# Kernel tuning notes

Hardware: AMD Instinct MI355X
Metric: run time of the kernel (lower is better)

## Reference

```python
import jax, jax.numpy as jnp
import numpy as np


def setup_inputs() -> dict:
    key = jax.random.key(0)
    k1, k2, k3, k4, k5 = jax.random.split(key, 5)
    B, S, IN, OUT, GS = 64, 1, 8192, 28672, 128
    n_groups = IN // GS  # 64
    return {
        "input": jax.random.normal(k1, (B, S, IN), dtype=jnp.float32),
        # packed int4 weights: two 4-bit values per byte along in_features
        "qweight": jax.random.randint(k2, (IN // 2, OUT), 0, 256, dtype=jnp.int32),
        # per-group scales (small positive, typical of quantized weights)
        "scales": (jax.random.uniform(k3, (n_groups, OUT), dtype=jnp.float32) * 0.01 + 1e-3),
        # per-group zero points, 4-bit range
        "qzeros": jax.random.randint(k4, (n_groups, OUT), 0, 16, dtype=jnp.int32),
        "bias": jax.random.normal(k5, (OUT,), dtype=jnp.float32),
        "group_size": GS,
    }


def _dequant_int4(qweight, scales, qzeros, group_size):
    # qweight: [in/2, out] bytes; low nibble = even k, high nibble = odd k
    half_in, out_f = qweight.shape
    in_f = half_in * 2
    lo = qweight & 0xF
    hi = (qweight >> 4) & 0xF
    # interleave nibbles along in_features -> [in, out]
    w_q = jnp.stack([lo, hi], axis=1).reshape(in_f, out_f).astype(scales.dtype)
    n_groups = scales.shape[0]
    # (q - zero) * scale, per group of `group_size` rows
    w = (w_q.reshape(n_groups, group_size, out_f)
         - qzeros.astype(scales.dtype)[:, None, :]) * scales[:, None, :]
    return w.reshape(in_f, out_f)


def reference(input, qweight, scales, qzeros, bias, group_size):
    # Fused dequant-int4 matmul (decode path, seq_len == 1): y = x @ W + b
    w = _dequant_int4(qweight, scales, qzeros, group_size)  # [in, out]
    return jnp.einsum('bsi,io->bso', input, w) + bias
```

## Files before the change

kernel.cpp:

```cpp
#include <hip/hip_runtime.h>
#include <hip/hip_bf16.h>


typedef float  f32x4 __attribute__((ext_vector_type(4)));
typedef float  f32x2 __attribute__((ext_vector_type(2)));
typedef short  s16x8 __attribute__((ext_vector_type(8)));
typedef int    i32x2 __attribute__((ext_vector_type(2)));
typedef int    i32x4 __attribute__((ext_vector_type(4)));

#define M_DIM 64
#define K_DIM 8192
#define N_DIM 28672
#define BN    64
#define CK    128
#define NCHUNK (K_DIM / CK)

__device__ s16x8 g_wsa[NCHUNK * 1024];

static __device__ __forceinline__ short f2bf(float f) {
    return (short)__builtin_bit_cast(unsigned short, __float2bfloat16(f));
}

__global__ __launch_bounds__(256)
void prep_a_kernel(const float* __restrict__ x) {
    const int tid = threadIdx.x;
    const int c   = blockIdx.x >> 2;
    const int mb  = blockIdx.x & 3;
    const int k8  = tid & 15;
    const int m   = mb * 16 + (tid >> 4);
    const float* src = x + (size_t)m * K_DIM + c * CK + k8 * 8;
    f32x4 a = *(const f32x4*)src;
    f32x4 b = *(const f32x4*)(src + 4);
    s16x8 o;
    o[0] = f2bf(a[0]); o[1] = f2bf(a[1]); o[2] = f2bf(a[2]); o[3] = f2bf(a[3]);
    o[4] = f2bf(b[0]); o[5] = f2bf(b[1]); o[6] = f2bf(b[2]); o[7] = f2bf(b[3]);
    g_wsa[(size_t)c * 1024 + k8 * 64 + m] = o;
}

__global__ __launch_bounds__(512, 4)
void int4gemm_kernel(const int*   __restrict__ qw,
                     const float* __restrict__ sc,
                     const int*   __restrict__ qz,
                     const float* __restrict__ bias,
                     float*       __restrict__ out)
{
    __shared__ s16x8 lB[16 * 64];
    __shared__ s16x8 lA[16 * 64];

    const int tid   = threadIdx.x;
    const int lane  = tid & 63;
    const int wave  = tid >> 6;
    const int nbase = blockIdx.x * BN;

    const int p  = tid & 31;
    const int q  = tid >> 5;
    const int j0 = nbase + 2 * p;

    const int l15 = lane & 15;
    const int lk  = lane >> 4;
    const int mh  = wave >> 2;
    const int wn  = (wave & 3) * 16;

    f32x4 acc0 = (f32x4)0.0f, acc1 = (f32x4)0.0f;

    const int* qbase = qw + j0;
    const i32x4* wsa4 = (const i32x4*)g_wsa;

    i32x2 bvA[4], bvB[4], bvN[4];
    i32x4 av0, av1;
    f32x2 sA, sB, sN;
    i32x2 zA, zB, zN;

#pragma unroll
    for (int r = 0; r < 4; ++r) {
        bvA[r] = *(const i32x2*)(qbase + (size_t)(q * 4 + r) * N_DIM);
        bvB[r] = *(const i32x2*)(qbase + (size_t)(64 + q * 4 + r) * N_DIM);
    }
    sA = *(const f32x2*)(sc + j0);
    sB = *(const f32x2*)(sc + N_DIM + j0);
    zA = *(const i32x2*)(qz + j0);
    zB = *(const i32x2*)(qz + N_DIM + j0);
    av0 = wsa4[tid];
    av1 = wsa4[512 + tid];

    for (int c = 0; c < NCHUNK; ++c) {
        const float s0 = sA.x, s1 = sA.y;
        const float o0 = -(float)zA.x * s0;
        const float o1 = -(float)zA.y * s1;
        s16x8 c0, c1;
#pragma unroll
        for (int r = 0; r < 4; ++r) {
            const int vx = bvA[r].x, vy = bvA[r].y;
            c0[2 * r]     = f2bf(fmaf((float)(vx & 15),        s0, o0));
            c0[2 * r + 1] = f2bf(fmaf((float)((vx >> 4) & 15), s0, o0));
            c1[2 * r]     = f2bf(fmaf((float)(vy & 15),        s1, o1));
            c1[2 * r + 1] = f2bf(fmaf((float)((vy >> 4) & 15), s1, o1));
        }

        asm volatile("s_barrier" ::: "memory");

        lB[q * 64 + 2 * p]     = c0;
        lB[q * 64 + 2 * p + 1] = c1;
        lA[tid]       = __builtin_bit_cast(s16x8, av0);
        lA[512 + tid] = __builtin_bit_cast(s16x8, av1);

        const int ca = (c + 1) & (NCHUNK - 1);
        av0 = wsa4[(size_t)ca * 1024 + tid];
        av1 = wsa4[(size_t)ca * 1024 + 512 + tid];
        const int cb = (c + 2) & (NCHUNK - 1);
#pragma unroll
        for (int r = 0; r < 4; ++r)
            bvN[r] = *(const i32x2*)(qbase + (size_t)(cb * 64 + q * 4 + r) * N_DIM);
        sN = *(const f32x2*)(sc + (size_t)cb * N_DIM + j0);
        zN = *(const i32x2*)(qz + (size_t)cb * N_DIM + j0);

        asm volatile("s_waitcnt lgkmcnt(0)" ::: "memory");
        asm volatile("s_barrier" ::: "memory");
        __builtin_amdgcn_sched_barrier(0);

#pragma unroll
        for (int ks = 0; ks < 4; ++ks) {
            const int cell = (ks * 4 + lk) * 64;
            const s16x8 bfr = lB[cell + wn + l15];
            const s16x8 af0 = lA[cell + mh * 32 + l15];
            const s16x8 af1 = lA[cell + mh * 32 + 16 + l15];
            acc0 = __builtin_amdgcn_mfma_f32_16x16x32_bf16(af0, bfr, acc0, 0, 0, 0);
            acc1 = __builtin_amdgcn_mfma_f32_16x16x32_bf16(af1, bfr, acc1, 0, 0, 0);
        }

#pragma unroll
        for (int r = 0; r < 4; ++r) { bvA[r] = bvB[r]; bvB[r] = bvN[r]; }
        sA = sB; sB = sN; zA = zB; zB = zN;
    }

    const int   ncol = nbase + wn + l15;
    const float bv   = bias[ncol];
    const int   m0   = mh * 32 + lk * 4;
#pragma unroll
    for (int jj = 0; jj < 4; ++jj) {
        out[(size_t)(m0 + jj) * N_DIM + ncol]      = acc0[jj] + bv;
        out[(size_t)(m0 + 16 + jj) * N_DIM + ncol] = acc1[jj] + bv;
    }
}

extern "C" void kernel_launch(void* const* d_in, const int* in_sizes, int n_in,
                              void* d_out, int out_size, void* d_ws, size_t ws_size,
                              hipStream_t stream) {
    const float* x    = (const float*)d_in[0];
    const int*   qw   = (const int*)d_in[1];
    const float* sc   = (const float*)d_in[2];
    const int*   qz   = (const int*)d_in[3];
    const float* bias = (const float*)d_in[4];
    float*       out  = (float*)d_out;

    prep_a_kernel<<<dim3(256), dim3(256), 0, stream>>>(x);
    int4gemm_kernel<<<dim3(N_DIM / BN), dim3(512), 0, stream>>>(qw, sc, qz, bias, out);
}
```

Baseline: 122.1 us.

## Restructure int4 GEMM to 4 waves with 2x2 MFMA tiles and double-buffered LDS

Cuts the block from 512 to 256 threads. Each wave now computes a 32x32 output tile with four accumulators, and A fragments are read straight from global memory into registers instead of staged through LDS. The B dequant tile is double-buffered in LDS so only one barrier per chunk is needed, and weight prefetch depth drops from two chunks to one with scalar per-column loads. This trades more registers and less load latency hiding for fewer barriers and less LDS traffic.

```diff
diff --git a/kernel.cpp b/kernel.cpp
--- a/kernel.cpp
+++ b/kernel.cpp
@@ -3,16 +3,13 @@
 
 
 typedef float  f32x4 __attribute__((ext_vector_type(4)));
-typedef float  f32x2 __attribute__((ext_vector_type(2)));
 typedef short  s16x8 __attribute__((ext_vector_type(8)));
-typedef int    i32x2 __attribute__((ext_vector_type(2)));
 typedef int    i32x4 __attribute__((ext_vector_type(4)));
 
-#define M_DIM 64
-#define K_DIM 8192
-#define N_DIM 28672
-#define BN    64
-#define CK    128
+#define K_DIM  8192
+#define N_DIM  28672
+#define BN     64
+#define CK     128
 #define NCHUNK (K_DIM / CK)
 
 __device__ s16x8 g_wsa[NCHUNK * 1024];
@@ -37,109 +34,114 @@
     g_wsa[(size_t)c * 1024 + k8 * 64 + m] = o;
 }
 
-__global__ __launch_bounds__(512, 4)
+__global__ __launch_bounds__(256, 3)
 void int4gemm_kernel(const int*   __restrict__ qw,
                      const float* __restrict__ sc,
                      const int*   __restrict__ qz,
                      const float* __restrict__ bias,
                      float*       __restrict__ out)
 {
-    __shared__ s16x8 lB[16 * 64];
-    __shared__ s16x8 lA[16 * 64];
+    __shared__ s16x8 lB[2][16 * 64];
 
     const int tid   = threadIdx.x;
     const int lane  = tid & 63;
-    const int wave  = tid >> 6;
+    const int w     = tid >> 6;
     const int nbase = blockIdx.x * BN;
 
-    const int p  = tid & 31;
-    const int q  = tid >> 5;
-    const int j0 = nbase + 2 * p;
+    const int col = lane;
 
     const int l15 = lane & 15;
     const int lk  = lane >> 4;
-    const int mh  = wave >> 2;
-    const int wn  = (wave & 3) * 16;
+    const int mh  = w >> 1;
+    const int nh  = w & 1;
 
-    f32x4 acc0 = (f32x4)0.0f, acc1 = (f32x4)0.0f;
+    const int*   qcol = qw + nbase + col;
+    const float* scol = sc + nbase + col;
+    const int*   zcol = qz + nbase + col;
 
-    const int* qbase = qw + j0;
-    const i32x4* wsa4 = (const i32x4*)g_wsa;
+    f32x4 acc[2][2];
+#pragma unroll
+    for (int mi = 0; mi < 2; ++mi)
+#pragma unroll
+        for (int ni = 0; ni < 2; ++ni) acc[mi][ni] = (f32x4)0.0f;
 
-    i32x2 bvA[4], bvB[4], bvN[4];
-    i32x4 av0, av1;
-    f32x2 sA, sB, sN;
-    i32x2 zA, zB, zN;
+    int   bvC[16], bvN[16];
+    float sC, sN_;
+    int   zC, zN_;
 
 #pragma unroll
-    for (int r = 0; r < 4; ++r) {
-        bvA[r] = *(const i32x2*)(qbase + (size_t)(q * 4 + r) * N_DIM);
-        bvB[r] = *(const i32x2*)(qbase + (size_t)(64 + q * 4 + r) * N_DIM);
-    }
-    sA = *(const f32x2*)(sc + j0);
-    sB = *(const f32x2*)(sc + N_DIM + j0);
-    zA = *(const i32x2*)(qz + j0);
-    zB = *(const i32x2*)(qz + N_DIM + j0);
-    av0 = wsa4[tid];
-    av1 = wsa4[512 + tid];
+    for (int u = 0; u < 16; ++u)
+        bvC[u] = qcol[(size_t)(16 * w + u) * N_DIM];
+    sC = scol[0];
+    zC = zcol[0];
+
+    const i32x4* wsa  = (const i32x4*)g_wsa;
+    const int    aoff = lk * 64 + mh * 32 + l15;
 
     for (int c = 0; c < NCHUNK; ++c) {
-        const float s0 = sA.x, s1 = sA.y;
-        const float o0 = -(float)zA.x * s0;
-        const float o1 = -(float)zA.y * s1;
-        s16x8 c0, c1;
+        const int cb = (c + 1) & (NCHUNK - 1);
+
 #pragma unroll
-        for (int r = 0; r < 4; ++r) {
-            const int vx = bvA[r].x, vy = bvA[r].y;
-            c0[2 * r]     = f2bf(fmaf((float)(vx & 15),        s0, o0));
-            c0[2 * r + 1] = f2bf(fmaf((float)((vx >> 4) & 15), s0, o0));
-            c1[2 * r]     = f2bf(fmaf((float)(vy & 15),        s1, o1));
-            c1[2 * r + 1] = f2bf(fmaf((float)((vy >> 4) & 15), s1, o1));
+        for (int u = 0; u < 16; ++u)
+            bvN[u] = qcol[(size_t)(cb * 64 + 16 * w + u) * N_DIM];
+        sN_ = scol[(size_t)cb * N_DIM];
+        zN_ = zcol[(size_t)cb * N_DIM];
+
+        i32x4 af[4][2];
+#pragma unroll
+        for (int ks = 0; ks < 4; ++ks)
+#pragma unroll
+            for (int mi = 0; mi < 2; ++mi)
+                af[ks][mi] = wsa[(size_t)c * 1024 + ks * 256 + mi * 16 + aoff];
+
+        const float s = sC;
+        const float o = -(float)zC * s;
+#pragma unroll
+        for (int jp = 0; jp < 4; ++jp) {
+            s16x8 cell;
+#pragma unroll
+            for (int uu = 0; uu < 4; ++uu) {
+                const int v = bvC[4 * jp + uu];
+                cell[2 * uu]     = f2bf(fmaf((float)(v & 15), s, o));
+                cell[2 * uu + 1] = f2bf(fmaf((float)(v >> 4), s, o));
+            }
+            lB[c & 1][(4 * w + jp) * 64 + col] = cell;
         }
-
-        asm volatile("s_barrier" ::: "memory");
-
-        lB[q * 64 + 2 * p]     = c0;
-        lB[q * 64 + 2 * p + 1] = c1;
-        lA[tid]       = __builtin_bit_cast(s16x8, av0);
-        lA[512 + tid] = __builtin_bit_cast(s16x8, av1);
-
-        const int ca = (c + 1) & (NCHUNK - 1);
-        av0 = wsa4[(size_t)ca * 1024 + tid];
-        av1 = wsa4[(size_t)ca * 1024 + 512 + tid];
-        const int cb = (c + 2) & (NCHUNK - 1);
-#pragma unroll
-        for (int r = 0; r < 4; ++r)
-            bvN[r] = *(const i32x2*)(qbase + (size_t)(cb * 64 + q * 4 + r) * N_DIM);
-        sN = *(const f32x2*)(sc + (size_t)cb * N_DIM + j0);
-        zN = *(const i32x2*)(qz + (size_t)cb * N_DIM + j0);
 
         asm volatile("s_waitcnt lgkmcnt(0)" ::: "memory");
         asm volatile("s_barrier" ::: "memory");
-        __builtin_amdgcn_sched_barrier(0);
 
 #pragma unroll
         for (int ks = 0; ks < 4; ++ks) {
-            const int cell = (ks * 4 + lk) * 64;
-            const s16x8 bfr = lB[cell + wn + l15];
-            const s16x8 af0 = lA[cell + mh * 32 + l15];
-            const s16x8 af1 = lA[cell + mh * 32 + 16 + l15];
-            acc0 = __builtin_amdgcn_mfma_f32_16x16x32_bf16(af0, bfr, acc0, 0, 0, 0);
-            acc1 = __builtin_amdgcn_mfma_f32_16x16x32_bf16(af1, bfr, acc1, 0, 0, 0);
+            const int cidx = (ks * 4 + lk) * 64 + nh * 32 + l15;
+            const s16x8 b0 = lB[c & 1][cidx];
+            const s16x8 b1 = lB[c & 1][cidx + 16];
+#pragma unroll
+            for (int mi = 0; mi < 2; ++mi) {
+                const s16x8 a = __builtin_bit_cast(s16x8, af[ks][mi]);
+                acc[mi][0] = __builtin_amdgcn_mfma_f32_16x16x32_bf16(a, b0, acc[mi][0], 0, 0, 0);
+                acc[mi][1] = __builtin_amdgcn_mfma_f32_16x16x32_bf16(a, b1, acc[mi][1], 0, 0, 0);
+            }
         }
 
 #pragma unroll
-        for (int r = 0; r < 4; ++r) { bvA[r] = bvB[r]; bvB[r] = bvN[r]; }
-        sA = sB; sB = sN; zA = zB; zB = zN;
+        for (int u = 0; u < 16; ++u) bvC[u] = bvN[u];
+        sC = sN_;
+        zC = zN_;
     }
 
-    const int   ncol = nbase + wn + l15;
-    const float bv   = bias[ncol];
-    const int   m0   = mh * 32 + lk * 4;
 #pragma unroll
-    for (int jj = 0; jj < 4; ++jj) {
-        out[(size_t)(m0 + jj) * N_DIM + ncol]      = acc0[jj] + bv;
-        out[(size_t)(m0 + 16 + jj) * N_DIM + ncol] = acc1[jj] + bv;
+    for (int ni = 0; ni < 2; ++ni) {
+        const int   ncol = nbase + nh * 32 + ni * 16 + l15;
+        const float bv   = bias[ncol];
+#pragma unroll
+        for (int mi = 0; mi < 2; ++mi) {
+#pragma unroll
+            for (int jj = 0; jj < 4; ++jj) {
+                const int m = mh * 32 + mi * 16 + lk * 4 + jj;
+                out[(size_t)m * N_DIM + ncol] = acc[mi][ni][jj] + bv;
+            }
+        }
     }
 }
 
@@ -154,5 +156,5 @@
     float*       out  = (float*)d_out;
 
     prep_a_kernel<<<dim3(256), dim3(256), 0, stream>>>(x);
-    int4gemm_kernel<<<dim3(N_DIM / BN), dim3(512), 0, stream>>>(qw, sc, qz, bias, out);
+    int4gemm_kernel<<<dim3(N_DIM / BN), dim3(256), 0, stream>>>(qw, sc, qz, bias, out);
 }
```

Result: slower. 143.6 us (+17.6%).

## Split K across four blocks and accumulate partial results with atomics

Applied to the files above, without the earlier changes.

Splits the K dimension into four ranges, each handled by its own block, so the grid grows from 448 to 1792 blocks. This fills the GPU's compute units better and gives more latency hiding for the weight-bandwidth-bound decode GEMM. Partial sums are combined with float atomicAdd into an output zeroed by a memset, and only the first split adds the bias. The cost is an extra memset, atomic traffic on the output, and a nondeterministic summation order.

```diff
diff --git a/kernel.cpp b/kernel.cpp
--- a/kernel.cpp
+++ b/kernel.cpp
@@ -13,7 +13,10 @@
 #define N_DIM 28672
 #define BN    64
 #define CK    128
-#define NCHUNK (K_DIM / CK)
+#define NCHUNK 64
+#define KSPLIT 4
+#define NCH_L  (NCHUNK / KSPLIT)
+#define NB     (N_DIM / BN)
 
 __device__ s16x8 g_wsa[NCHUNK * 1024];
 
@@ -50,7 +53,10 @@
     const int tid   = threadIdx.x;
     const int lane  = tid & 63;
     const int wave  = tid >> 6;
-    const int nbase = blockIdx.x * BN;
+    const int nb    = blockIdx.x % NB;
+    const int ksp   = blockIdx.x / NB;
+    const int kbase = ksp * NCH_L;
+    const int nbase = nb * BN;
 
     const int p  = tid & 31;
     const int q  = tid >> 5;
@@ -73,17 +79,18 @@
 
 #pragma unroll
     for (int r = 0; r < 4; ++r) {
-        bvA[r] = *(const i32x2*)(qbase + (size_t)(q * 4 + r) * N_DIM);
-        bvB[r] = *(const i32x2*)(qbase + (size_t)(64 + q * 4 + r) * N_DIM);
+        bvA[r] = *(const i32x2*)(qbase + (size_t)((kbase)     * 64 + q * 4 + r) * N_DIM);
+        bvB[r] = *(const i32x2*)(qbase + (size_t)((kbase + 1) * 64 + q * 4 + r) * N_DIM);
     }
-    sA = *(const f32x2*)(sc + j0);
-    sB = *(const f32x2*)(sc + N_DIM + j0);
-    zA = *(const i32x2*)(qz + j0);
-    zB = *(const i32x2*)(qz + N_DIM + j0);
-    av0 = wsa4[tid];
-    av1 = wsa4[512 + tid];
+    sA = *(const f32x2*)(sc + (size_t)kbase * N_DIM + j0);
+    sB = *(const f32x2*)(sc + (size_t)(kbase + 1) * N_DIM + j0);
+    zA = *(const i32x2*)(qz + (size_t)kbase * N_DIM + j0);
+    zB = *(const i32x2*)(qz + (size_t)(kbase + 1) * N_DIM + j0);
+    av0 = wsa4[(size_t)kbase * 1024 + tid];
+    av1 = wsa4[(size_t)kbase * 1024 + 512 + tid];
 
-    for (int c = 0; c < NCHUNK; ++c) {
+#pragma unroll 2
+    for (int c = 0; c < NCH_L; ++c) {
         const float s0 = sA.x, s1 = sA.y;
         const float o0 = -(float)zA.x * s0;
         const float o1 = -(float)zA.y * s1;
@@ -99,15 +106,15 @@
 
         asm volatile("s_barrier" ::: "memory");
 
-        lB[q * 64 + 2 * p]     = c0;
-        lB[q * 64 + 2 * p + 1] = c1;
+        lB[q * 64 + 2 * p]          = c0;
+        lB[q * 64 + 2 * p + 1]      = c1;
         lA[tid]       = __builtin_bit_cast(s16x8, av0);
         lA[512 + tid] = __builtin_bit_cast(s16x8, av1);
 
-        const int ca = (c + 1) & (NCHUNK - 1);
+        const int ca = kbase + ((c + 1 < NCH_L) ? c + 1 : NCH_L - 1);
         av0 = wsa4[(size_t)ca * 1024 + tid];
         av1 = wsa4[(size_t)ca * 1024 + 512 + tid];
-        const int cb = (c + 2) & (NCHUNK - 1);
+        const int cb = kbase + ((c + 2 < NCH_L) ? c + 2 : NCH_L - 1);
 #pragma unroll
         for (int r = 0; r < 4; ++r)
             bvN[r] = *(const i32x2*)(qbase + (size_t)(cb * 64 + q * 4 + r) * N_DIM);
@@ -134,12 +141,12 @@
     }
 
     const int   ncol = nbase + wn + l15;
-    const float bv   = bias[ncol];
+    const float bv   = (ksp == 0) ? bias[ncol] : 0.0f;
     const int   m0   = mh * 32 + lk * 4;
 #pragma unroll
     for (int jj = 0; jj < 4; ++jj) {
-        out[(size_t)(m0 + jj) * N_DIM + ncol]      = acc0[jj] + bv;
-        out[(size_t)(m0 + 16 + jj) * N_DIM + ncol] = acc1[jj] + bv;
+        atomicAdd(&out[(size_t)(m0 + jj) * N_DIM + ncol],      acc0[jj] + bv);
+        atomicAdd(&out[(size_t)(m0 + 16 + jj) * N_DIM + ncol], acc1[jj] + bv);
     }
 }
 
@@ -153,6 +160,7 @@
     const float* bias = (const float*)d_in[4];
     float*       out  = (float*)d_out;
 
+    hipMemsetAsync(d_out, 0, (size_t)out_size * sizeof(float), stream);
     prep_a_kernel<<<dim3(256), dim3(256), 0, stream>>>(x);
-    int4gemm_kernel<<<dim3(N_DIM / BN), dim3(512), 0, stream>>>(qw, sc, qz, bias, out);
+    int4gemm_kernel<<<dim3(NB * KSPLIT), dim3(512), 0, stream>>>(qw, sc, qz, bias, out);
 }
```

Measured after the change: 132.2 us. 1.08x slower.
